# Kernel optimization log

Measured on AMD Instinct MI355X. Metric: run time of the kernel, lower is better.

Reference implementation:

```python
import jax, jax.numpy as jnp
import numpy as np


def setup_inputs() -> dict:
    key = jax.random.key(0)
    k1, k2 = jax.random.split(key)
    B, S, V = 8, 512, 30522
    logits = jax.random.normal(k1, (B, S, V), dtype=jnp.float32)
    attention_mask = jax.random.randint(k2, (B, S), 0, 2, dtype=jnp.int32)
    return {"logits": logits, "attention_mask": attention_mask, "top_k": 64}


def reference(logits, attention_mask, top_k):
    # Fused SPLADE activation: log1p(relu(logits)) * mask, max-pooled over seq.
    mask = attention_mask.astype(logits.dtype)[:, :, None]        # (B, S, 1)
    activated = jnp.log1p(jax.nn.relu(logits)) * mask             # (B, S, V)
    values = jnp.max(activated, axis=1)                           # (B, V)
    # Top-k thresholding: zero out everything below the k-th largest value.
    top_values, _ = jax.lax.top_k(values, top_k)                  # (B, k)
    threshold = top_values[..., -1, None]                         # (B, 1)
    return values * (values >= threshold).astype(values.dtype)
```

## Files before the change

kernel.cpp:

```cpp
#include <hip/hip_runtime.h>
#include <hip/hip_bf16.h>

constexpr int B_ = 8;
constexpr int S_ = 512;
constexpr int V_ = 30522;

constexpr int K1_BLOCK = 256;
constexpr int K1_VEC   = 2;
constexpr int K1_COLS  = K1_BLOCK * K1_VEC;
constexpr int NVCHUNK  = (V_ + K1_COLS - 1) / K1_COLS;

__global__ __launch_bounds__(K1_BLOCK)
void splade_max_kernel(const float* __restrict__ logits,
                       const int* __restrict__ mask,
                       float* __restrict__ out)
{
    __shared__ int s_idx[S_];
    __shared__ int s_cnt;
    const int b = blockIdx.y;

    if (threadIdx.x == 0) s_cnt = 0;
    __syncthreads();
    for (int i = threadIdx.x; i < S_; i += K1_BLOCK)
        if (mask[b * S_ + i] != 0)
            s_idx[atomicAdd(&s_cnt, 1)] = i;
    __syncthreads();
    const int n = s_cnt;

    const int c0 = (blockIdx.x * K1_BLOCK + threadIdx.x) * K1_VEC;
    if (c0 >= V_) return;

    const float* base = logits + (size_t)b * S_ * V_ + c0;
    float m0 = 0.0f, m1 = 0.0f;

    int j = 0;
    for (; j + 8 <= n; j += 8) {
        const int i0 = s_idx[j+0], i1 = s_idx[j+1], i2 = s_idx[j+2], i3 = s_idx[j+3];
        const int i4 = s_idx[j+4], i5 = s_idx[j+5], i6 = s_idx[j+6], i7 = s_idx[j+7];
        const float2 x0 = *reinterpret_cast<const float2*>(base + (size_t)i0 * V_);
        const float2 x1 = *reinterpret_cast<const float2*>(base + (size_t)i1 * V_);
        const float2 x2 = *reinterpret_cast<const float2*>(base + (size_t)i2 * V_);
        const float2 x3 = *reinterpret_cast<const float2*>(base + (size_t)i3 * V_);
        const float2 x4 = *reinterpret_cast<const float2*>(base + (size_t)i4 * V_);
        const float2 x5 = *reinterpret_cast<const float2*>(base + (size_t)i5 * V_);
        const float2 x6 = *reinterpret_cast<const float2*>(base + (size_t)i6 * V_);
        const float2 x7 = *reinterpret_cast<const float2*>(base + (size_t)i7 * V_);
        m0 = fmaxf(m0, fmaxf(fmaxf(fmaxf(x0.x, x1.x), fmaxf(x2.x, x3.x)),
                             fmaxf(fmaxf(x4.x, x5.x), fmaxf(x6.x, x7.x))));
        m1 = fmaxf(m1, fmaxf(fmaxf(fmaxf(x0.y, x1.y), fmaxf(x2.y, x3.y)),
                             fmaxf(fmaxf(x4.y, x5.y), fmaxf(x6.y, x7.y))));
    }
    for (; j < n; ++j) {
        const float2 x = *reinterpret_cast<const float2*>(base + (size_t)s_idx[j] * V_);
        m0 = fmaxf(m0, x.x);
        m1 = fmaxf(m1, x.y);
    }
    *reinterpret_cast<float2*>(out + (size_t)b * V_ + c0) = make_float2(m0, m1);
}

constexpr int K2_BLOCK = 1024;
constexpr int NPT = (V_ + K2_BLOCK - 1) / K2_BLOCK;

__global__ __launch_bounds__(K2_BLOCK)
void splade_topk_kernel(float* __restrict__ vals,
                        const int* __restrict__ topk_ptr)
{
    const int b = blockIdx.x;
    const int k = topk_ptr[0];
    float* row = vals + (size_t)b * V_;

    unsigned int v[NPT];
#pragma unroll
    for (int i = 0; i < NPT; ++i) {
        const int idx = threadIdx.x + i * K2_BLOCK;
        v[i] = (idx < V_) ? __float_as_uint(row[idx]) : 0u;
    }

    __shared__ int s_cnt;
    unsigned int lo = 0u, hi = 0x7f800000u;
    while (hi - lo > 1u) {
        const unsigned int mid = lo + ((hi - lo) >> 1);
        int c = 0;
#pragma unroll
        for (int i = 0; i < NPT; ++i)
            c += (v[i] >= mid) ? 1 : 0;
        for (int off = 32; off > 0; off >>= 1)
            c += __shfl_down(c, off);
        if (threadIdx.x == 0) s_cnt = 0;
        __syncthreads();
        if ((threadIdx.x & 63) == 0) atomicAdd(&s_cnt, c);
        __syncthreads();
        const int cnt = s_cnt;
        if (cnt >= k) lo = mid; else hi = mid;
        __syncthreads();
    }

    const unsigned int T = lo;
#pragma unroll
    for (int i = 0; i < NPT; ++i) {
        const int idx = threadIdx.x + i * K2_BLOCK;
        if (idx < V_) {
            const float m = __uint_as_float(v[i]);
            row[idx] = (v[i] >= T) ? log1pf(m) : 0.0f;
        }
    }
}

extern "C" void kernel_launch(void* const* d_in, const int* in_sizes, int n_in,
                              void* d_out, int out_size, void* d_ws, size_t ws_size,
                              hipStream_t stream) {
    const float* logits = (const float*)d_in[0];
    const int*   mask   = (const int*)d_in[1];
    const int*   topk   = (const int*)d_in[2];
    float*       out    = (float*)d_out;

    dim3 g1(NVCHUNK, B_);
    splade_max_kernel<<<g1, K1_BLOCK, 0, stream>>>(logits, mask, out);
    splade_topk_kernel<<<B_, K2_BLOCK, 0, stream>>>(out, topk);
}
```

Before: 84.00 us.

## Use nontemporal loads, ballot-based mask compaction, and leaner top-k bisection

The max-pooling kernel now reads logits with nontemporal loads and issues 16 loads per unrolled step instead of 8, aiming for more memory-level parallelism on a pass that streams about 1 GB. Mask compaction moves from shared-memory atomics to a single-wave ballot/popcount scan, which also keeps token order deterministic. The top-k kernel drops to 256 threads, loads and stores float2 pairs, counts with ballot+popcount, and gives each bisection iteration its own shared counter to remove two barriers per step. In exchange, register pressure rises in both kernels and the top-k kernel runs with less parallelism per row.

```diff
diff --git a/kernel.cpp b/kernel.cpp
--- a/kernel.cpp
+++ b/kernel.cpp
@@ -4,6 +4,15 @@
 constexpr int B_ = 8;
 constexpr int S_ = 512;
 constexpr int V_ = 30522;
+
+static __device__ __forceinline__ float2 ntload2(const float* p) {
+    const unsigned long long u =
+        __builtin_nontemporal_load(reinterpret_cast<const unsigned long long*>(p));
+    float2 r;
+    r.x = __uint_as_float((unsigned int)u);
+    r.y = __uint_as_float((unsigned int)(u >> 32));
+    return r;
+}
 
 constexpr int K1_BLOCK = 256;
 constexpr int K1_VEC   = 2;
@@ -19,11 +28,17 @@
     __shared__ int s_cnt;
     const int b = blockIdx.y;
 
-    if (threadIdx.x == 0) s_cnt = 0;
-    __syncthreads();
-    for (int i = threadIdx.x; i < S_; i += K1_BLOCK)
-        if (mask[b * S_ + i] != 0)
-            s_idx[atomicAdd(&s_cnt, 1)] = i;
+    if (threadIdx.x < 64) {
+        const int lane = threadIdx.x;
+        int cnt = 0;
+        for (int base = 0; base < S_; base += 64) {
+            const int m = mask[b * S_ + base + lane] != 0;
+            const unsigned long long bal = __ballot(m);
+            if (m) s_idx[cnt + (int)__popcll(bal & ((1ull << lane) - 1ull))] = base + lane;
+            cnt += (int)__popcll(bal);
+        }
+        if (lane == 0) s_cnt = cnt;
+    }
     __syncthreads();
     const int n = s_cnt;
 
@@ -34,32 +49,28 @@
     float m0 = 0.0f, m1 = 0.0f;
 
     int j = 0;
-    for (; j + 8 <= n; j += 8) {
-        const int i0 = s_idx[j+0], i1 = s_idx[j+1], i2 = s_idx[j+2], i3 = s_idx[j+3];
-        const int i4 = s_idx[j+4], i5 = s_idx[j+5], i6 = s_idx[j+6], i7 = s_idx[j+7];
-        const float2 x0 = *reinterpret_cast<const float2*>(base + (size_t)i0 * V_);
-        const float2 x1 = *reinterpret_cast<const float2*>(base + (size_t)i1 * V_);
-        const float2 x2 = *reinterpret_cast<const float2*>(base + (size_t)i2 * V_);
-        const float2 x3 = *reinterpret_cast<const float2*>(base + (size_t)i3 * V_);
-        const float2 x4 = *reinterpret_cast<const float2*>(base + (size_t)i4 * V_);
-        const float2 x5 = *reinterpret_cast<const float2*>(base + (size_t)i5 * V_);
-        const float2 x6 = *reinterpret_cast<const float2*>(base + (size_t)i6 * V_);
-        const float2 x7 = *reinterpret_cast<const float2*>(base + (size_t)i7 * V_);
-        m0 = fmaxf(m0, fmaxf(fmaxf(fmaxf(x0.x, x1.x), fmaxf(x2.x, x3.x)),
-                             fmaxf(fmaxf(x4.x, x5.x), fmaxf(x6.x, x7.x))));
-        m1 = fmaxf(m1, fmaxf(fmaxf(fmaxf(x0.y, x1.y), fmaxf(x2.y, x3.y)),
-                             fmaxf(fmaxf(x4.y, x5.y), fmaxf(x6.y, x7.y))));
+    for (; j + 16 <= n; j += 16) {
+        float2 x[16];
+#pragma unroll
+        for (int u = 0; u < 16; ++u)
+            x[u] = ntload2(base + (size_t)s_idx[j + u] * V_);
+#pragma unroll
+        for (int u = 0; u < 16; ++u) {
+            m0 = fmaxf(m0, x[u].x);
+            m1 = fmaxf(m1, x[u].y);
+        }
     }
     for (; j < n; ++j) {
-        const float2 x = *reinterpret_cast<const float2*>(base + (size_t)s_idx[j] * V_);
+        const float2 x = ntload2(base + (size_t)s_idx[j] * V_);
         m0 = fmaxf(m0, x.x);
         m1 = fmaxf(m1, x.y);
     }
     *reinterpret_cast<float2*>(out + (size_t)b * V_ + c0) = make_float2(m0, m1);
 }
 
-constexpr int K2_BLOCK = 1024;
-constexpr int NPT = (V_ + K2_BLOCK - 1) / K2_BLOCK;
+constexpr int K2_BLOCK = 256;
+constexpr int V2   = V_ / 2;
+constexpr int NPT2 = (V2 + K2_BLOCK - 1) / K2_BLOCK;
 
 __global__ __launch_bounds__(K2_BLOCK)
 void splade_topk_kernel(float* __restrict__ vals,
@@ -69,39 +80,48 @@
     const int k = topk_ptr[0];
     float* row = vals + (size_t)b * V_;
 
-    unsigned int v[NPT];
+    unsigned int v[2 * NPT2];
 #pragma unroll
-    for (int i = 0; i < NPT; ++i) {
-        const int idx = threadIdx.x + i * K2_BLOCK;
-        v[i] = (idx < V_) ? __float_as_uint(row[idx]) : 0u;
+    for (int i = 0; i < NPT2; ++i) {
+        const int idx2 = threadIdx.x + i * K2_BLOCK;
+        if (idx2 < V2) {
+            const float2 x = *reinterpret_cast<const float2*>(row + 2 * idx2);
+            v[2 * i]     = __float_as_uint(x.x);
+            v[2 * i + 1] = __float_as_uint(x.y);
+        } else {
+            v[2 * i] = 0u;
+            v[2 * i + 1] = 0u;
+        }
     }
 
-    __shared__ int s_cnt;
+    __shared__ int s_cnt[32];
+    for (int i = threadIdx.x; i < 32; i += K2_BLOCK) s_cnt[i] = 0;
+    __syncthreads();
+
     unsigned int lo = 0u, hi = 0x7f800000u;
-    while (hi - lo > 1u) {
+    for (int it = 0; it < 32; ++it) {
+        if (hi - lo <= 1u) break;
         const unsigned int mid = lo + ((hi - lo) >> 1);
         int c = 0;
 #pragma unroll
-        for (int i = 0; i < NPT; ++i)
-            c += (v[i] >= mid) ? 1 : 0;
-        for (int off = 32; off > 0; off >>= 1)
-            c += __shfl_down(c, off);
-        if (threadIdx.x == 0) s_cnt = 0;
+        for (int i = 0; i < 2 * NPT2; ++i)
+            c += (int)__popcll(__ballot(v[i] >= mid));
+        if ((threadIdx.x & 63) == 0) atomicAdd(&s_cnt[it], c);
         __syncthreads();
-        if ((threadIdx.x & 63) == 0) atomicAdd(&s_cnt, c);
-        __syncthreads();
-        const int cnt = s_cnt;
+        const int cnt = s_cnt[it];
         if (cnt >= k) lo = mid; else hi = mid;
-        __syncthreads();
     }
 
     const unsigned int T = lo;
 #pragma unroll
-    for (int i = 0; i < NPT; ++i) {
-        const int idx = threadIdx.x + i * K2_BLOCK;
-        if (idx < V_) {
-            const float m = __uint_as_float(v[i]);
-            row[idx] = (v[i] >= T) ? log1pf(m) : 0.0f;
+    for (int i = 0; i < NPT2; ++i) {
+        const int idx2 = threadIdx.x + i * K2_BLOCK;
+        if (idx2 < V2) {
+            const unsigned int a = v[2 * i], c = v[2 * i + 1];
+            float rx = 0.0f, ry = 0.0f;
+            if (a >= T) rx = log1pf(__uint_as_float(a));
+            if (c >= T) ry = log1pf(__uint_as_float(c));
+            *reinterpret_cast<float2*>(row + 2 * idx2) = make_float2(rx, ry);
         }
     }
 }
```

Measured after the change: 147.6 us. 75.7% more time.

## Split sequence reduction across blocks and streamline top-k threshold search

Applied to the files above, without the earlier changes.

The max-pooling kernel now splits the sequence dimension into four chunks, giving four times as many blocks. Each chunk writes a partial max into the output or workspace, and the top-k kernel merges the four partials. Mask compaction now uses a wavefront ballot and prefix popcount instead of shared atomics. The binary search counts with ballot/popcount and uses a separate shared counter per iteration, which drops two barriers per step. The cost is extra workspace traffic and the partial-max merge inside the single-block-per-row top-k kernel.

```diff
diff --git a/kernel.cpp b/kernel.cpp
--- a/kernel.cpp
+++ b/kernel.cpp
@@ -9,28 +9,39 @@
 constexpr int K1_VEC   = 2;
 constexpr int K1_COLS  = K1_BLOCK * K1_VEC;
 constexpr int NVCHUNK  = (V_ + K1_COLS - 1) / K1_COLS;
+constexpr int NSCHUNK  = 4;
+constexpr int SCHUNK   = S_ / NSCHUNK;
 
 __global__ __launch_bounds__(K1_BLOCK)
 void splade_max_kernel(const float* __restrict__ logits,
                        const int* __restrict__ mask,
-                       float* __restrict__ out)
+                       float* __restrict__ out,
+                       float* __restrict__ ws)
 {
-    __shared__ int s_idx[S_];
+    __shared__ int s_idx[SCHUNK];
     __shared__ int s_cnt;
-    const int b = blockIdx.y;
+    const int sc = blockIdx.y;
+    const int b  = blockIdx.z;
+    const int s0 = sc * SCHUNK;
 
-    if (threadIdx.x == 0) s_cnt = 0;
-    __syncthreads();
-    for (int i = threadIdx.x; i < S_; i += K1_BLOCK)
-        if (mask[b * S_ + i] != 0)
-            s_idx[atomicAdd(&s_cnt, 1)] = i;
+    if (threadIdx.x < 64) {
+        const int lane = threadIdx.x;
+        int cnt = 0;
+        for (int base = 0; base < SCHUNK; base += 64) {
+            const int m = mask[b * S_ + s0 + base + lane] != 0;
+            const unsigned long long bal = __ballot(m);
+            if (m) s_idx[cnt + (int)__popcll(bal & ((1ull << lane) - 1ull))] = base + lane;
+            cnt += (int)__popcll(bal);
+        }
+        if (lane == 0) s_cnt = cnt;
+    }
     __syncthreads();
     const int n = s_cnt;
 
     const int c0 = (blockIdx.x * K1_BLOCK + threadIdx.x) * K1_VEC;
     if (c0 >= V_) return;
 
-    const float* base = logits + (size_t)b * S_ * V_ + c0;
+    const float* base = logits + (size_t)(b * S_ + s0) * V_ + c0;
     float m0 = 0.0f, m1 = 0.0f;
 
     int j = 0;
@@ -55,44 +66,51 @@
         m0 = fmaxf(m0, x.x);
         m1 = fmaxf(m1, x.y);
     }
-    *reinterpret_cast<float2*>(out + (size_t)b * V_ + c0) = make_float2(m0, m1);
+    float* dst = (sc == 0) ? out : ws + (size_t)(sc - 1) * B_ * V_;
+    *reinterpret_cast<float2*>(dst + (size_t)b * V_ + c0) = make_float2(m0, m1);
 }
 
 constexpr int K2_BLOCK = 1024;
 constexpr int NPT = (V_ + K2_BLOCK - 1) / K2_BLOCK;
 
 __global__ __launch_bounds__(K2_BLOCK)
-void splade_topk_kernel(float* __restrict__ vals,
+void splade_topk_kernel(float* __restrict__ out,
+                        const float* __restrict__ ws,
                         const int* __restrict__ topk_ptr)
 {
     const int b = blockIdx.x;
     const int k = topk_ptr[0];
-    float* row = vals + (size_t)b * V_;
+    float* row = out + (size_t)b * V_;
+    const float* p1 = ws + (size_t)b * V_;
+    const float* p2 = ws + (size_t)(B_ + b) * V_;
+    const float* p3 = ws + (size_t)(2 * B_ + b) * V_;
 
     unsigned int v[NPT];
 #pragma unroll
     for (int i = 0; i < NPT; ++i) {
         const int idx = threadIdx.x + i * K2_BLOCK;
-        v[i] = (idx < V_) ? __float_as_uint(row[idx]) : 0u;
+        float m = 0.0f;
+        if (idx < V_)
+            m = fmaxf(fmaxf(row[idx], p1[idx]), fmaxf(p2[idx], p3[idx]));
+        v[i] = __float_as_uint(m);
     }
 
-    __shared__ int s_cnt;
+    __shared__ int s_cnt[32];
+    for (int i = threadIdx.x; i < 32; i += K2_BLOCK) s_cnt[i] = 0;
+    __syncthreads();
+
     unsigned int lo = 0u, hi = 0x7f800000u;
-    while (hi - lo > 1u) {
+    for (int it = 0; it < 32; ++it) {
+        if (hi - lo <= 1u) break;
         const unsigned int mid = lo + ((hi - lo) >> 1);
         int c = 0;
 #pragma unroll
         for (int i = 0; i < NPT; ++i)
-            c += (v[i] >= mid) ? 1 : 0;
-        for (int off = 32; off > 0; off >>= 1)
-            c += __shfl_down(c, off);
-        if (threadIdx.x == 0) s_cnt = 0;
+            c += (int)__popcll(__ballot(v[i] >= mid));
+        if ((threadIdx.x & 63) == 0) atomicAdd(&s_cnt[it], c);
         __syncthreads();
-        if ((threadIdx.x & 63) == 0) atomicAdd(&s_cnt, c);
-        __syncthreads();
-        const int cnt = s_cnt;
+        const int cnt = s_cnt[it];
         if (cnt >= k) lo = mid; else hi = mid;
-        __syncthreads();
     }
 
     const unsigned int T = lo;
@@ -113,8 +131,9 @@
     const int*   mask   = (const int*)d_in[1];
     const int*   topk   = (const int*)d_in[2];
     float*       out    = (float*)d_out;
+    float*       ws     = (float*)d_ws;
 
-    dim3 g1(NVCHUNK, B_);
-    splade_max_kernel<<<g1, K1_BLOCK, 0, stream>>>(logits, mask, out);
-    splade_topk_kernel<<<B_, K2_BLOCK, 0, stream>>>(out, topk);
+    dim3 g1(NVCHUNK, NSCHUNK, B_);
+    splade_max_kernel<<<g1, K1_BLOCK, 0, stream>>>(logits, mask, out, ws);
+    splade_topk_kernel<<<B_, K2_BLOCK, 0, stream>>>(out, ws, topk);
 }
```

Measured after the change: 97.32 us. 1.16x slower.
